# Optimization experiments

Measured on AMD Instinct MI355X. Metric: run time of the kernel, lower is better.

Reference implementation:

```python
import jax, jax.numpy as jnp
import numpy as np

H = 12          # num_attention_heads
D = 64          # num_embed_hidden == attention_head_size
B, T = 4, 2048
SCALE = 1.0 / np.sqrt(D)


def setup_inputs() -> dict:
    key = jax.random.key(0)
    ks = jax.random.split(key, 7)
    P = H * D  # num_attn_proj = 768
    s = 1.0 / np.sqrt(D)
    return {
        "hidden_states": jax.random.normal(ks[0], (B, T, D), dtype=jnp.float32),
        "attention_mask": jnp.ones((B, T), dtype=jnp.float32),
        "Wq": jax.random.normal(ks[1], (D, P), dtype=jnp.float32) * s,
        "bq": jnp.zeros((P,), dtype=jnp.float32),
        "Wk": jax.random.normal(ks[2], (D, P), dtype=jnp.float32) * s,
        "bk": jnp.zeros((P,), dtype=jnp.float32),
        "Wv": jax.random.normal(ks[3], (D, P), dtype=jnp.float32) * s,
        "bv": jnp.zeros((P,), dtype=jnp.float32),
    }


def reference(hidden_states, attention_mask, Wq, bq, Wk, bk, Wv, bv):
    b, t, _ = hidden_states.shape
    # QKV projections -> [B, H, T, D]
    def proj(W, bias):
        return (hidden_states @ W + bias).reshape(b, t, H, D).transpose(0, 2, 1, 3)
    q = proj(Wq, bq)
    k = proj(Wk, bk)
    v = proj(Wv, bv)
    # [B, H, T, T] scores
    scores = jnp.einsum("bhqd,bhkd->bhqk", q, k) * SCALE
    mask = (1.0 - attention_mask)[:, None, None, :] * -10000.0
    scores = scores + mask
    attn = jax.nn.softmax(scores, axis=-1)
    # dropout is identity in eval mode
    y = jnp.einsum("bhqk,bhkd->bhqd", attn, v)
    return y.transpose(0, 2, 1, 3).reshape(b, t, H * D)
```

## Files before the change

kernel.cpp:

```cpp
#include <hip/hip_runtime.h>
#include <hip/hip_bf16.h>

#define NH 12
#define HD 64
#define NB 4
#define SEQ 2048
#define NP 768
#define LOG2E 1.44269504f
#define MASK_L2 14426.9504f

typedef __bf16 bf16x8 __attribute__((ext_vector_type(8)));
typedef float f32x4 __attribute__((ext_vector_type(4)));
typedef float f32x16 __attribute__((ext_vector_type(16)));
typedef unsigned u32x4 __attribute__((ext_vector_type(4)));

static __device__ __forceinline__ bf16x8 load_bf16x8(const __bf16* p) {
    return *reinterpret_cast<const bf16x8*>(p);
}
static __device__ __forceinline__ float hw_exp2(float x) {
    return __builtin_amdgcn_exp2f(x);
}
static __device__ __forceinline__ unsigned pack_bf16(float lo, float hi) {
    unsigned a = (unsigned)__builtin_bit_cast(unsigned short, (__bf16)lo);
    unsigned b = (unsigned)__builtin_bit_cast(unsigned short, (__bf16)hi);
    return a | (b << 16);
}

__global__ __launch_bounds__(256) void qkv_kernel(
    const float* __restrict__ hidden,
    const float* __restrict__ Wq, const float* __restrict__ Wk,
    const float* __restrict__ Wv,
    const float* __restrict__ bq, const float* __restrict__ bk,
    const float* __restrict__ bv,
    __bf16* __restrict__ Qw, __bf16* __restrict__ Kf, __bf16* __restrict__ Vf)
{
    __shared__ __bf16 wtileT[64][72];
    __shared__ __bf16 ot[64][72];

    const int tid  = threadIdx.x;
    const int lane = tid & 63;
    const int w    = tid >> 6;
    const int g    = lane >> 4;
    const int n    = lane & 15;
    const int n32  = lane & 31;
    const int hi   = lane >> 5;

    const int row0 = blockIdx.x * 64;
    const int gi   = blockIdx.y;
    const int b_   = row0 >> 11;
    const int t0   = row0 & (SEQ - 1);
    const int kb64 = t0 >> 6;

    const float* hrow = hidden + (size_t)(row0 + w * 16 + n) * HD + 8 * g;
    f32x4 h0 = *(const f32x4*)(hrow);
    f32x4 h1 = *(const f32x4*)(hrow + 4);
    f32x4 h2 = *(const f32x4*)(hrow + 32);
    f32x4 h3 = *(const f32x4*)(hrow + 36);
    bf16x8 a0, a1;
    #pragma unroll
    for (int j = 0; j < 4; ++j) {
        a0[j]     = (__bf16)h0[j];
        a0[j + 4] = (__bf16)h1[j];
        a1[j]     = (__bf16)h2[j];
        a1[j + 4] = (__bf16)h3[j];
    }

    const int dr   = tid >> 2;
    const int coff = (tid & 3) * 16;

    for (int tt = 0; tt < 6; ++tt) {
        const int tile_id = gi * 6 + tt;
        const int proj    = tile_id / 12;
        const int head    = tile_id % 12;
        const int bh      = b_ * NH + head;
        const float* W    = proj == 0 ? Wq : (proj == 1 ? Wk : Wv);
        const float* bias = proj == 0 ? bq : (proj == 1 ? bk : bv);
        const float qs    = (proj == 0) ? 0.125f * LOG2E : 1.0f;

        const float* wr = W + (size_t)dr * NP + head * 64 + coff;
        f32x4 x0 = *(const f32x4*)(wr);
        f32x4 x1 = *(const f32x4*)(wr + 4);
        f32x4 x2 = *(const f32x4*)(wr + 8);
        f32x4 x3 = *(const f32x4*)(wr + 12);
        #pragma unroll
        for (int i = 0; i < 4; ++i) {
            wtileT[coff + i     ][dr] = (__bf16)(x0[i] * qs);
            wtileT[coff + 4 + i ][dr] = (__bf16)(x1[i] * qs);
            wtileT[coff + 8 + i ][dr] = (__bf16)(x2[i] * qs);
            wtileT[coff + 12 + i][dr] = (__bf16)(x3[i] * qs);
        }
        __syncthreads();

        #pragma unroll
        for (int dt = 0; dt < 4; ++dt) {
            const bf16x8 b0 = *(const bf16x8*)&wtileT[dt * 16 + n][8 * g];
            const bf16x8 b1 = *(const bf16x8*)&wtileT[dt * 16 + n][32 + 8 * g];
            f32x4 acc = {0.f, 0.f, 0.f, 0.f};
            acc = __builtin_amdgcn_mfma_f32_16x16x32_bf16(a0, b0, acc, 0, 0, 0);
            acc = __builtin_amdgcn_mfma_f32_16x16x32_bf16(a1, b1, acc, 0, 0, 0);
            const float bb = bias[head * 64 + dt * 16 + n] * qs;
            #pragma unroll
            for (int r = 0; r < 4; ++r)
                ot[w * 16 + 4 * g + r][dt * 16 + n] = (__bf16)(acc[r] + bb);
        }
        __syncthreads();

        if (proj == 0) {
            __bf16* dst = Qw + ((size_t)bh * SEQ + t0 + w * 16) * HD;
            const int tr = lane >> 2;
            const int d0 = (lane & 3) * 16;
            *(bf16x8*)(dst + (size_t)tr * HD + d0)     = *(const bf16x8*)&ot[w * 16 + tr][d0];
            *(bf16x8*)(dst + (size_t)tr * HD + d0 + 8) = *(const bf16x8*)&ot[w * 16 + tr][d0 + 8];
        } else if (proj == 1) {
            __bf16* base = Kf + (size_t)bh * SEQ * HD + (size_t)kb64 * 4096;
            #pragma unroll
            for (int sub = 0; sub < 2; ++sub) {
                const bf16x8 fr = *(const bf16x8*)&ot[sub * 32 + n32][w * 16 + 8 * hi];
                *(bf16x8*)(base + (size_t)(w * 2 + sub) * 512 + lane * 8) = fr;
            }
        } else {
            __bf16* base = Vf + (size_t)bh * SEQ * HD + (size_t)kb64 * 4096;
            #pragma unroll
            for (int dsub = 0; dsub < 2; ++dsub) {
                bf16x8 v;
                #pragma unroll
                for (int j = 0; j < 8; ++j)
                    v[j] = ot[w * 16 + 8 * hi + j][dsub * 32 + n32];
                *(bf16x8*)(base + (size_t)(w * 2 + dsub) * 512 + lane * 8) = v;
            }
        }
    }
}

__global__ __launch_bounds__(256, 3) void flash_attn_kernel(
    const __bf16* __restrict__ Qw, const __bf16* __restrict__ Kf,
    const __bf16* __restrict__ Vf, const float* __restrict__ amask,
    float* __restrict__ out)
{
    __shared__ __align__(16) float et[4][32][68];
    __shared__ float lrow[4][32];
    __shared__ __bf16 mdd[SEQ];

    const int tid  = threadIdx.x;
    const int lane = tid & 63;
    const int w    = tid >> 6;
    const int n32  = lane & 31;
    const int hi   = lane >> 5;

    const int bid    = blockIdx.x;
    const int xcd    = bid & 7;
    const int slot   = bid >> 3;
    const int bh     = xcd * 6 + (slot >> 6);
    const int qchunk = slot & 63;
    const int b_     = bh / NH;
    const int h      = bh % NH;
    const int q0     = qchunk * 32;

    const float* mp = amask + (size_t)b_ * SEQ;
    #pragma unroll
    for (int i = 0; i < 8; ++i) {
        const int idx = w * 512 + i * 64 + lane;
        mdd[idx] = (__bf16)fmaf(mp[idx], MASK_L2, -MASK_L2);
    }

    const __bf16* Qrow = Qw + ((size_t)bh * SEQ + q0 + n32) * HD + 8 * hi;
    bf16x8 qf[4];
    #pragma unroll
    for (int d = 0; d < 4; ++d) qf[d] = load_bf16x8(Qrow + d * 16);

    bf16x8 qone;
    #pragma unroll
    for (int j = 0; j < 8; ++j) qone[j] = (__bf16)0.0f;
    if (hi == 0) qone[0] = (__bf16)1.0f;

    const __bf16* kfb_ = Kf + (size_t)bh * SEQ * HD + (size_t)lane * 8;
    const __bf16* vfb_ = Vf + (size_t)bh * SEQ * HD + (size_t)lane * 8;

    f32x16 o0 = {0,0,0,0,0,0,0,0,0,0,0,0,0,0,0,0};
    f32x16 o1 = {0,0,0,0,0,0,0,0,0,0,0,0,0,0,0,0};
    float lsl = 0.f;

    const int kstart = w * 512;
    for (int it = 0; it < 8; ++it) {
        const int kb = kstart + it * 64;
        const size_t foff = (size_t)(kb >> 6) * 4096;

        bf16x8 kfa[4], kfb[4];
        #pragma unroll
        for (int d = 0; d < 4; ++d) {
            kfa[d] = load_bf16x8(kfb_ + foff + (size_t)(2 * d) * 512);
            kfb[d] = load_bf16x8(kfb_ + foff + (size_t)(2 * d + 1) * 512);
        }

        bf16x8 maa, mab;
        #pragma unroll
        for (int j = 0; j < 8; ++j) { maa[j] = (__bf16)0.0f; mab[j] = (__bf16)0.0f; }
        maa[0] = mdd[kb + n32];
        mab[0] = mdd[kb + 32 + n32];

        f32x16 sa = {0,0,0,0,0,0,0,0,0,0,0,0,0,0,0,0};
        f32x16 sb = {0,0,0,0,0,0,0,0,0,0,0,0,0,0,0,0};
        #pragma unroll
        for (int d = 0; d < 4; ++d) {
            sa = __builtin_amdgcn_mfma_f32_32x32x16_bf16(kfa[d], qf[d], sa, 0, 0, 0);
            sb = __builtin_amdgcn_mfma_f32_32x32x16_bf16(kfb[d], qf[d], sb, 0, 0, 0);
        }
        sa = __builtin_amdgcn_mfma_f32_32x32x16_bf16(maa, qone, sa, 0, 0, 0);
        sb = __builtin_amdgcn_mfma_f32_32x32x16_bf16(mab, qone, sb, 0, 0, 0);

        bf16x8 vf0[4], vf1[4];
        #pragma unroll
        for (int k = 0; k < 4; ++k) {
            vf0[k] = load_bf16x8(vfb_ + foff + (size_t)(2 * k) * 512);
            vf1[k] = load_bf16x8(vfb_ + foff + (size_t)(2 * k + 1) * 512);
        }

        bf16x8 pA0, pA1, pB0, pB1;
        #pragma unroll
        for (int half = 0; half < 2; ++half) {
            const f32x16& s = half ? sb : sa;
            float p[16];
            #pragma unroll
            for (int r = 0; r < 16; ++r) { p[r] = hw_exp2(s[r]); lsl += p[r]; }
            unsigned pk[8], xp[8];
            #pragma unroll
            for (int i = 0; i < 8; ++i) pk[i] = pack_bf16(p[2 * i], p[2 * i + 1]);
            #pragma unroll
            for (int i = 0; i < 8; ++i) xp[i] = __shfl_xor(pk[i], 32);
            u32x4 B0, B1;
            B0[0] = hi ? xp[2] : pk[0];  B0[1] = hi ? xp[3] : pk[1];
            B0[2] = hi ? pk[2] : xp[0];  B0[3] = hi ? pk[3] : xp[1];
            B1[0] = hi ? xp[6] : pk[4];  B1[1] = hi ? xp[7] : pk[5];
            B1[2] = hi ? pk[6] : xp[4];  B1[3] = hi ? pk[7] : xp[5];
            if (half == 0) { pA0 = __builtin_bit_cast(bf16x8, B0); pA1 = __builtin_bit_cast(bf16x8, B1); }
            else           { pB0 = __builtin_bit_cast(bf16x8, B0); pB1 = __builtin_bit_cast(bf16x8, B1); }
        }

        o0 = __builtin_amdgcn_mfma_f32_32x32x16_bf16(vf0[0], pA0, o0, 0, 0, 0);
        o0 = __builtin_amdgcn_mfma_f32_32x32x16_bf16(vf0[1], pA1, o0, 0, 0, 0);
        o0 = __builtin_amdgcn_mfma_f32_32x32x16_bf16(vf0[2], pB0, o0, 0, 0, 0);
        o0 = __builtin_amdgcn_mfma_f32_32x32x16_bf16(vf0[3], pB1, o0, 0, 0, 0);
        o1 = __builtin_amdgcn_mfma_f32_32x32x16_bf16(vf1[0], pA0, o1, 0, 0, 0);
        o1 = __builtin_amdgcn_mfma_f32_32x32x16_bf16(vf1[1], pA1, o1, 0, 0, 0);
        o1 = __builtin_amdgcn_mfma_f32_32x32x16_bf16(vf1[2], pB0, o1, 0, 0, 0);
        o1 = __builtin_amdgcn_mfma_f32_32x32x16_bf16(vf1[3], pB1, o1, 0, 0, 0);
    }

    const float rs = lsl + __shfl_xor(lsl, 32);

    #pragma unroll
    for (int r = 0; r < 16; ++r) {
        const int dl = (r & 3) + 8 * (r >> 2) + 4 * hi;
        et[w][n32][dl]      = o0[r];
        et[w][n32][32 + dl] = o1[r];
    }
    if (lane < 32) lrow[w][n32] = rs;
    __syncthreads();

    const int q  = tid >> 3;
    const int d0 = (tid & 7) * 8;
    const float linv = 1.0f / (lrow[0][q] + lrow[1][q] + lrow[2][q] + lrow[3][q]);
    f32x4 acc0 = {0,0,0,0}, acc1 = {0,0,0,0};
    #pragma unroll
    for (int ww = 0; ww < 4; ++ww) {
        acc0 += *(const f32x4*)&et[ww][q][d0];
        acc1 += *(const f32x4*)&et[ww][q][d0 + 4];
    }
    float* orow = out + ((size_t)(b_ * SEQ + q0 + q)) * NP + h * HD + d0;
    f32x4 r0, r1;
    #pragma unroll
    for (int i = 0; i < 4; ++i) { r0[i] = acc0[i] * linv; r1[i] = acc1[i] * linv; }
    *(f32x4*)(orow)     = r0;
    *(f32x4*)(orow + 4) = r1;
}

extern "C" void kernel_launch(void* const* d_in, const int* in_sizes, int n_in,
                              void* d_out, int out_size, void* d_ws, size_t ws_size,
                              hipStream_t stream) {
    const float* hidden = (const float*)d_in[0];
    const float* amask  = (const float*)d_in[1];
    const float* Wq     = (const float*)d_in[2];
    const float* bq     = (const float*)d_in[3];
    const float* Wk     = (const float*)d_in[4];
    const float* bk     = (const float*)d_in[5];
    const float* Wv     = (const float*)d_in[6];
    const float* bv     = (const float*)d_in[7];
    float* out = (float*)d_out;

    const size_t elems = (size_t)NB * NH * SEQ * HD;
    __bf16* Qw = (__bf16*)d_ws;
    __bf16* Kf = Qw + elems;
    __bf16* Vf = Kf + elems;

    qkv_kernel<<<dim3(128, 6), 256, 0, stream>>>(
        hidden, Wq, Wk, Wv, bq, bk, bv, Qw, Kf, Vf);

    flash_attn_kernel<<<dim3(3072), 256, 0, stream>>>(
        Qw, Kf, Vf, amask, out);
}
```

Before: 177.4 us.

## Permute V fragment layout to drop P shuffles and compute row sums via MFMA

The V projection writer now stores keys in the permuted order that matches the MFMA accumulator layout of P, so the softmax probabilities can be packed straight into B operands without cross-lane shuffles and selects. Row sums of P are no longer accumulated with scalar adds; an extra MFMA against an all-ones A operand accumulates them in a matrix register, and row sums now come from the bf16-rounded P values. V loads are hoisted next to the K loads, and the loop is unrolled by 2. Launch bounds drop from 3 to 2 waves per SIMD to leave room for the added registers, which may lower occupancy.

Result: slower. 190.9 us (+7.6%).

```diff
diff --git a/kernel.cpp b/kernel.cpp
--- a/kernel.cpp
+++ b/kernel.cpp
@@ -125,14 +125,14 @@
                 bf16x8 v;
                 #pragma unroll
                 for (int j = 0; j < 8; ++j)
-                    v[j] = ot[w * 16 + 8 * hi + j][dsub * 32 + n32];
+                    v[j] = ot[w * 16 + ((j & 3) + 8 * (j >> 2) + 4 * hi)][dsub * 32 + n32];
                 *(bf16x8*)(base + (size_t)(w * 2 + dsub) * 512 + lane * 8) = v;
             }
         }
     }
 }
 
-__global__ __launch_bounds__(256, 3) void flash_attn_kernel(
+__global__ __launch_bounds__(256, 2) void flash_attn_kernel(
     const __bf16* __restrict__ Qw, const __bf16* __restrict__ Kf,
     const __bf16* __restrict__ Vf, const float* __restrict__ amask,
     float* __restrict__ out)
@@ -168,19 +168,20 @@
     #pragma unroll
     for (int d = 0; d < 4; ++d) qf[d] = load_bf16x8(Qrow + d * 16);
 
-    bf16x8 qone;
-    #pragma unroll
-    for (int j = 0; j < 8; ++j) qone[j] = (__bf16)0.0f;
+    bf16x8 qone, aones;
+    #pragma unroll
+    for (int j = 0; j < 8; ++j) { qone[j] = (__bf16)0.0f; aones[j] = (__bf16)1.0f; }
     if (hi == 0) qone[0] = (__bf16)1.0f;
 
     const __bf16* kfb_ = Kf + (size_t)bh * SEQ * HD + (size_t)lane * 8;
     const __bf16* vfb_ = Vf + (size_t)bh * SEQ * HD + (size_t)lane * 8;
 
-    f32x16 o0 = {0,0,0,0,0,0,0,0,0,0,0,0,0,0,0,0};
-    f32x16 o1 = {0,0,0,0,0,0,0,0,0,0,0,0,0,0,0,0};
-    float lsl = 0.f;
+    f32x16 o0   = {0,0,0,0,0,0,0,0,0,0,0,0,0,0,0,0};
+    f32x16 o1   = {0,0,0,0,0,0,0,0,0,0,0,0,0,0,0,0};
+    f32x16 lacc = {0,0,0,0,0,0,0,0,0,0,0,0,0,0,0,0};
 
     const int kstart = w * 512;
+    #pragma unroll 2
     for (int it = 0; it < 8; ++it) {
         const int kb = kstart + it * 64;
         const size_t foff = (size_t)(kb >> 6) * 4096;
@@ -191,6 +192,12 @@
             kfa[d] = load_bf16x8(kfb_ + foff + (size_t)(2 * d) * 512);
             kfb[d] = load_bf16x8(kfb_ + foff + (size_t)(2 * d + 1) * 512);
         }
+        bf16x8 vf0[4], vf1[4];
+        #pragma unroll
+        for (int c = 0; c < 4; ++c) {
+            vf0[c] = load_bf16x8(vfb_ + foff + (size_t)(2 * c) * 512);
+            vf1[c] = load_bf16x8(vfb_ + foff + (size_t)(2 * c + 1) * 512);
+        }
 
         bf16x8 maa, mab;
         #pragma unroll
@@ -208,45 +215,34 @@
         sa = __builtin_amdgcn_mfma_f32_32x32x16_bf16(maa, qone, sa, 0, 0, 0);
         sb = __builtin_amdgcn_mfma_f32_32x32x16_bf16(mab, qone, sb, 0, 0, 0);
 
-        bf16x8 vf0[4], vf1[4];
-        #pragma unroll
-        for (int k = 0; k < 4; ++k) {
-            vf0[k] = load_bf16x8(vfb_ + foff + (size_t)(2 * k) * 512);
-            vf1[k] = load_bf16x8(vfb_ + foff + (size_t)(2 * k + 1) * 512);
-        }
-
-        bf16x8 pA0, pA1, pB0, pB1;
+        bf16x8 P[4];
         #pragma unroll
         for (int half = 0; half < 2; ++half) {
             const f32x16& s = half ? sb : sa;
             float p[16];
             #pragma unroll
-            for (int r = 0; r < 16; ++r) { p[r] = hw_exp2(s[r]); lsl += p[r]; }
-            unsigned pk[8], xp[8];
-            #pragma unroll
-            for (int i = 0; i < 8; ++i) pk[i] = pack_bf16(p[2 * i], p[2 * i + 1]);
-            #pragma unroll
-            for (int i = 0; i < 8; ++i) xp[i] = __shfl_xor(pk[i], 32);
+            for (int r = 0; r < 16; ++r) p[r] = hw_exp2(s[r]);
             u32x4 B0, B1;
-            B0[0] = hi ? xp[2] : pk[0];  B0[1] = hi ? xp[3] : pk[1];
-            B0[2] = hi ? pk[2] : xp[0];  B0[3] = hi ? pk[3] : xp[1];
-            B1[0] = hi ? xp[6] : pk[4];  B1[1] = hi ? xp[7] : pk[5];
-            B1[2] = hi ? pk[6] : xp[4];  B1[3] = hi ? pk[7] : xp[5];
-            if (half == 0) { pA0 = __builtin_bit_cast(bf16x8, B0); pA1 = __builtin_bit_cast(bf16x8, B1); }
-            else           { pB0 = __builtin_bit_cast(bf16x8, B0); pB1 = __builtin_bit_cast(bf16x8, B1); }
-        }
-
-        o0 = __builtin_amdgcn_mfma_f32_32x32x16_bf16(vf0[0], pA0, o0, 0, 0, 0);
-        o0 = __builtin_amdgcn_mfma_f32_32x32x16_bf16(vf0[1], pA1, o0, 0, 0, 0);
-        o0 = __builtin_amdgcn_mfma_f32_32x32x16_bf16(vf0[2], pB0, o0, 0, 0, 0);
-        o0 = __builtin_amdgcn_mfma_f32_32x32x16_bf16(vf0[3], pB1, o0, 0, 0, 0);
-        o1 = __builtin_amdgcn_mfma_f32_32x32x16_bf16(vf1[0], pA0, o1, 0, 0, 0);
-        o1 = __builtin_amdgcn_mfma_f32_32x32x16_bf16(vf1[1], pA1, o1, 0, 0, 0);
-        o1 = __builtin_amdgcn_mfma_f32_32x32x16_bf16(vf1[2], pB0, o1, 0, 0, 0);
-        o1 = __builtin_amdgcn_mfma_f32_32x32x16_bf16(vf1[3], pB1, o1, 0, 0, 0);
-    }
-
-    const float rs = lsl + __shfl_xor(lsl, 32);
+            #pragma unroll
+            for (int i = 0; i < 4; ++i) {
+                B0[i] = pack_bf16(p[2 * i],     p[2 * i + 1]);
+                B1[i] = pack_bf16(p[8 + 2 * i], p[8 + 2 * i + 1]);
+            }
+            P[2 * half]     = __builtin_bit_cast(bf16x8, B0);
+            P[2 * half + 1] = __builtin_bit_cast(bf16x8, B1);
+        }
+
+        lacc = __builtin_amdgcn_mfma_f32_32x32x16_bf16(aones, P[0], lacc, 0, 0, 0);
+        lacc = __builtin_amdgcn_mfma_f32_32x32x16_bf16(aones, P[1], lacc, 0, 0, 0);
+        lacc = __builtin_amdgcn_mfma_f32_32x32x16_bf16(aones, P[2], lacc, 0, 0, 0);
+        lacc = __builtin_amdgcn_mfma_f32_32x32x16_bf16(aones, P[3], lacc, 0, 0, 0);
+
+        #pragma unroll
+        for (int c = 0; c < 4; ++c) {
+            o0 = __builtin_amdgcn_mfma_f32_32x32x16_bf16(vf0[c], P[c], o0, 0, 0, 0);
+            o1 = __builtin_amdgcn_mfma_f32_32x32x16_bf16(vf1[c], P[c], o1, 0, 0, 0);
+        }
+    }
 
     #pragma unroll
     for (int r = 0; r < 16; ++r) {
@@ -254,7 +250,7 @@
         et[w][n32][dl]      = o0[r];
         et[w][n32][32 + dl] = o1[r];
     }
-    if (lane < 32) lrow[w][n32] = rs;
+    if (lane < 32) lrow[w][n32] = lacc[0];
     __syncthreads();
 
     const int q  = tid >> 3;
```
